# Kernel optimization log

Hardware: AMD Instinct MI355X
Metric: run time of the kernel (lower is better)

Reference implementation:

```python
import jax, jax.numpy as jnp
import numpy as np

G = 4      # groups (conv groups == offset groups)
KS = 3     # kernel size
DIL = 1    # dilation
PAD = 1    # padding = dilation
EPS = 1e-5 # InstanceNorm eps


def setup_inputs() -> dict:
    key = jax.random.key(0)
    k1, k2, k3, k4, k5 = jax.random.split(key, 5)
    B, C, D, H, W = 4, 64, 8, 64, 64
    Cout = 64
    Cg = C // G
    x = jax.random.normal(k1, (B, C, D, H, W), jnp.float32)
    # small offset-conv weights so predicted offsets stay within a few pixels
    w_off = jax.random.normal(k2, (2 * KS * KS * G, Cg, KS, KS), jnp.float32) * 0.01
    b_off = jax.random.normal(k3, (2 * KS * KS * G,), jnp.float32) * 0.01
    w_dc = jax.random.normal(k4, (Cout, Cg, KS, KS), jnp.float32) * (1.0 / np.sqrt(Cg * KS * KS))
    b_dc = jax.random.normal(k5, (Cout,), jnp.float32) * 0.01
    return {"x": x, "w_off": w_off, "b_off": b_off, "w_dc": w_dc, "b_dc": b_dc}


def reference(x, w_off, b_off, w_dc, b_dc):
    B, C, D, H, W = x.shape
    N = B * D
    K = KS * KS
    Cg = C // G
    # torch .view(B*D, C, H, W) is a row-major reshape of the flat buffer
    x2 = x.reshape(N, C, H, W)

    # grouped 3x3 offset conv, same padding
    off = jax.lax.conv_general_dilated(
        x2, w_off, (1, 1), [(PAD, PAD), (PAD, PAD)],
        rhs_dilation=(DIL, DIL), feature_group_count=G,
        dimension_numbers=("NCHW", "OIHW", "NCHW"),
    ) + b_off[None, :, None, None]
    off = off.reshape(N, G, K, 2, H, W)        # (y, x) offset per group/kernel-pt
    dy, dx = off[:, :, :, 0], off[:, :, :, 1]  # [N,G,K,H,W]

    # base sampling grid per kernel point
    ki, kj = jnp.meshgrid(jnp.arange(KS), jnp.arange(KS), indexing="ij")
    ki = ki.reshape(K); kj = kj.reshape(K)
    base_y = (jnp.arange(H)[None, :] - PAD + ki[:, None] * DIL).astype(jnp.float32)  # [K,H]
    base_x = (jnp.arange(W)[None, :] - PAD + kj[:, None] * DIL).astype(jnp.float32)  # [K,W]
    py = base_y[None, None, :, :, None] + dy   # [N,G,K,H,W]
    px = base_x[None, None, :, None, :] + dx

    y0 = jnp.floor(py); x0 = jnp.floor(px)
    ly = py - y0; lx = px - x0
    y0i = y0.astype(jnp.int32); x0i = x0.astype(jnp.int32)

    xg = x2.reshape(N, G, Cg, H * W)
    gather = jax.vmap(jax.vmap(lambda xf, idx: xf[:, idx]))  # over N, G

    def corner(yi, xi, w):
        valid = (yi >= 0) & (yi < H) & (xi >= 0) & (xi < W)   # zero-pad OOB
        idx = jnp.clip(yi, 0, H - 1) * W + jnp.clip(xi, 0, W - 1)
        v = gather(xg, idx.reshape(N, G, -1)).reshape(N, G, Cg, K, H, W)
        return v * (w * valid)[:, :, None]                    # broadcast over Cg

    val = (corner(y0i,     x0i,     (1 - ly) * (1 - lx))
         + corner(y0i,     x0i + 1, (1 - ly) * lx)
         + corner(y0i + 1, x0i,     ly * (1 - lx))
         + corner(y0i + 1, x0i + 1, ly * lx))                 # [N,G,Cg,K,H,W]

    wg = w_dc.reshape(G, -1, Cg, K)                           # [G,Coutg,Cg,K]
    out = jnp.einsum("gock,ngckhw->ngohw", wg, val).reshape(N, -1, H, W)
    out = out + b_dc[None, :, None, None]

    # InstanceNorm2d (affine=False, biased var) + exact GELU
    m = out.mean((-2, -1), keepdims=True)
    v = out.var((-2, -1), keepdims=True)
    out = jax.nn.gelu((out - m) * jax.lax.rsqrt(v + EPS), approximate=False)

    Cout = out.shape[1]
    return out.reshape(B, D, Cout, H, W).transpose(0, 2, 1, 3, 4)  # [B,Cout,D,H,W]
```

## Files before the change

kernel.cpp:

```cpp
#include <hip/hip_runtime.h>
#include <hip/hip_bf16.h>
#include <math.h>

#define HW 4096
#define NN 32
#define W68 68
#define SLICE (68 * 68)

typedef __attribute__((ext_vector_type(8))) short bf16x8;
typedef __attribute__((ext_vector_type(4))) float f32x4;

__device__ inline unsigned short bfbits(float a) {
    __hip_bfloat16 h = __float2bfloat16(a);
    unsigned short u;
    __builtin_memcpy(&u, &h, 2);
    return u;
}
__device__ inline unsigned packbf(float a, float b) {
    return (unsigned)bfbits(a) | ((unsigned)bfbits(b) << 16);
}
__device__ inline float bflo(unsigned u) { return __uint_as_float(u << 16); }
__device__ inline float bfhi(unsigned u) { return __uint_as_float(u & 0xffff0000u); }

__device__ inline int xsw(int x, int c8) {
    return ((x << 5) | (c8 << 4)) ^ (((x >> 2) & 1) << 4);
}

__device__ inline void bilin8(uint4 A, uint4 B, uint4 C, uint4 D,
                              const float* ww, float* val) {
    const unsigned* ua = (const unsigned*)&A;
    const unsigned* ub = (const unsigned*)&B;
    const unsigned* uc = (const unsigned*)&C;
    const unsigned* ud = (const unsigned*)&D;
    #pragma unroll
    for (int j = 0; j < 4; j++) {
        val[2*j]   = ww[0]*bflo(ua[j]) + ww[1]*bflo(ub[j]) + ww[2]*bflo(uc[j]) + ww[3]*bflo(ud[j]);
        val[2*j+1] = ww[0]*bfhi(ua[j]) + ww[1]*bfhi(ub[j]) + ww[2]*bfhi(uc[j]) + ww[3]*bfhi(ud[j]);
    }
}

__global__ __launch_bounds__(256) void transpose_x(const float* __restrict__ x,
                                                   unsigned short* __restrict__ xT,
                                                   const float* __restrict__ w_off,
                                                   const float* __restrict__ w_dc,
                                                   unsigned short* __restrict__ wperm)
{
    int bx = blockIdx.x;
    int t = threadIdx.x;

    if (bx < 120) {
        int idx = bx * 256 + t;
        int g = idx / 7680;
        int r3 = idx - g * 7680;
        int which = r3 / 2560;
        int r = r3 - which * 2560;
        int j = r & 7;
        int rest = r >> 3;
        int nn_ = rest & 15; rest >>= 4;
        int q_ = rest & 3, kp_ = rest >> 2;
        int k = q_ * 8 + j;
        int c = k & 15, tt = kp_ * 2 + (k >> 4);
        float v = 0.f;
        if (tt < 9) {
            if (which == 0)      v = w_dc[(g * 16 + nn_) * 144 + c * 9 + tt];
            else if (which == 1) v = w_off[(g * 18 + nn_) * 144 + c * 9 + tt];
            else if (nn_ < 2)    v = w_off[(g * 18 + 16 + nn_) * 144 + c * 9 + tt];
        }
        wperm[idx] = bfbits(v);
    }

    __shared__ float tile[256 * 17];
    int n = bx >> 6, g = (bx >> 4) & 3, chunk = bx & 15;
    const float* xb = x + (size_t)(n * 64 + g * 16) * HW + chunk * 256;

    #pragma unroll
    for (int r = 0; r < 16; r++) {
        int idx = r * 256 + t;
        int c = idx >> 8, p = idx & 255;
        tile[p * 17 + c] = xb[c * HW + p];
    }
    __syncthreads();

    unsigned short* ob = xT + (size_t)(n * 4 + g) * SLICE * 16;
    #pragma unroll
    for (int r = 0; r < 2; r++) {
        int idx = r * 256 + t;
        int p = idx >> 1, half = idx & 1;
        int pos = chunk * 256 + p;
        int h = pos >> 6, w = pos & 63;
        const float* tp = &tile[p * 17 + half * 8];
        uint4 v;
        v.x = packbf(tp[0], tp[1]);
        v.y = packbf(tp[2], tp[3]);
        v.z = packbf(tp[4], tp[5]);
        v.w = packbf(tp[6], tp[7]);
        *(uint4*)(ob + ((size_t)((h + 2) * W68 + (w + 2)) * 16 + half * 8)) = v;
    }

    if (t < 66) {
        int j = t >> 1, half = t & 1;
        int hp = chunk * 33 + j;
        int R, C;
        if (hp < 136)      { R = hp / 68;               C = hp % 68; }
        else if (hp < 272) { int q2 = hp - 136; R = 66 + q2 / 68; C = q2 % 68; }
        else               { int q2 = hp - 272; R = 2 + (q2 >> 2);
                             C = (q2 & 3); C = C < 2 ? C : C + 64; }
        uint4 z = {0, 0, 0, 0};
        *(uint4*)(ob + ((size_t)(R * W68 + C) * 16 + half * 8)) = z;
    }
}

__global__ __launch_bounds__(256, 4) void fused_conv(const unsigned short* __restrict__ xT,
                                                     const unsigned short* __restrict__ wperm,
                                                     const float* __restrict__ b_off,
                                                     const float* __restrict__ b_dc,
                                                     float* __restrict__ outpre)
{
    __shared__ __attribute__((aligned(16))) unsigned short xwin[9 * 1088];
    __shared__ __attribute__((aligned(8)))  unsigned short off_lds[256 * 20];

    int bx = blockIdx.x;
    int n = bx >> 6, g = (bx >> 4) & 3, chunk = bx & 15;
    int t = threadIdx.x;
    int lane = t & 63, wv = t >> 6;
    int nn = lane & 15, q = lane >> 4;
    int t2 = q >> 1, chh = q & 1;
    int R0 = chunk * 4;

    const unsigned short* wpg = wperm + g * 7680;
    const unsigned short* xsl = xT + (size_t)(n * 4 + g) * SLICE * 16;
    const unsigned short* xw  = xsl + chh * 8;

    {
        uint4 sv[5]; int sof[5];
        #pragma unroll
        for (int k = 0; k < 5; k++) {
            int sidx = k * 256 + t;
            int row = sidx / 136;
            int rem = sidx - row * 136;
            int xx = rem >> 1, c8 = rem & 1;
            int Rg = R0 + row; Rg = Rg > 67 ? 67 : Rg;
            bool ok = sidx < 1224;
            uint4 z = {0, 0, 0, 0};
            sv[k] = ok ? *(const uint4*)(xsl + ((size_t)(Rg * 68 + xx) * 16 + c8 * 8)) : z;
            sof[k] = row * 2176 + xsw(xx, c8);
        }
        #pragma unroll
        for (int k = 0; k < 5; k++) {
            int sidx = k * 256 + t;
            if (sidx < 1224)
                *(uint4*)((char*)xwin + sof[k]) = sv[k];
        }
    }

    int pls[4]; float fy[4], fx[4]; int rws[4], xbs[4];
    #pragma unroll
    for (int s = 0; s < 4; s++) {
        int pl = (wv * 4 + s) * 16 + nn;
        int pos = chunk * 256 + pl;
        int h = pos >> 6, w = pos & 63;
        pls[s] = pl;
        fy[s] = (float)(h - 1);
        fx[s] = (float)(w - 1);
        rws[s] = ((wv * 4 + s) >> 2) + 1;
        xbs[s] = ((wv * 4 + s) & 3) * 16 + nn + 1;
    }

    bf16x8 pb0[5], pb1[5], bwr[5];
    #pragma unroll
    for (int kp = 0; kp < 5; kp++) {
        int fo = ((kp * 4 + q) * 16 + nn) * 8;
        pb0[kp] = *(const bf16x8*)(wpg + 2560 + fo);
        pb1[kp] = *(const bf16x8*)(wpg + 5120 + fo);
        bwr[kp] = *(const bf16x8*)(wpg + fo);
    }

    __syncthreads();

    {
        f32x4 acc0[4], acc1[4];
        float bv0 = b_off[g * 18 + nn];
        float bv1 = (nn < 2) ? b_off[g * 18 + 16 + nn] : 0.f;
        #pragma unroll
        for (int s = 0; s < 4; s++)
            #pragma unroll
            for (int r = 0; r < 4; r++) { acc0[s][r] = bv0; acc1[s][r] = bv1; }

        uint4 xv[2][4];
        auto stage1 = [&](int kp) {
            int ki = t2 ? (2 * kp + 1) / 3 : (2 * kp) / 3;
            int kj = t2 ? (2 * kp + 1) % 3 : (2 * kp) % 3;
            int sl = kp & 1;
            #pragma unroll
            for (int s = 0; s < 4; s++) {
                int adr = (rws[s] + ki) * 2176 + xsw(xbs[s] + kj, chh);
                xv[sl][s] = *(const uint4*)((const char*)xwin + adr);
            }
        };
        stage1(0);
        #pragma unroll
        for (int kp = 0; kp < 5; kp++) {
            if (kp < 4) stage1(kp + 1);
            int sl = kp & 1;
            #pragma unroll
            for (int s = 0; s < 4; s++) {
                bf16x8 af = *(bf16x8*)&xv[sl][s];
                acc0[s] = __builtin_amdgcn_mfma_f32_16x16x32_bf16(af, pb0[kp], acc0[s], 0, 0, 0);
                acc1[s] = __builtin_amdgcn_mfma_f32_16x16x32_bf16(af, pb1[kp], acc1[s], 0, 0, 0);
            }
        }

        #pragma unroll
        for (int s = 0; s < 4; s++) {
            int pl = (wv * 4 + s) * 16 + q * 4;
            #pragma unroll
            for (int r = 0; r < 4; r++) {
                off_lds[(pl + r) * 20 + nn] = bfbits(acc0[s][r]);
                if (nn < 2)
                    off_lds[(pl + r) * 20 + 16 + nn] = bfbits(acc1[s][r]);
            }
        }
        off_lds[t * 20 + 18] = 0;
        off_lds[t * 20 + 19] = 0;
    }
    __syncthreads();

    f32x4 acc[4];
    float bv = b_dc[g * 16 + nn];
    #pragma unroll
    for (int s = 0; s < 4; s++)
        #pragma unroll
        for (int r = 0; r < 4; r++) acc[s][r] = bv;

    uint4 RA[2], RB[2], RC[2], RD[2];
    float rw_[2][4];
    int rinw[2], rgb[2];

    auto stage = [&](int u) {
        int kp = u >> 2, s = u & 3, sl = u & 1;
        int ki = t2 ? (2 * kp + 1) / 3 : (2 * kp) / 3;
        int kj = t2 ? (2 * kp + 1) % 3 : (2 * kp) % 3;
        unsigned uo = *(const unsigned*)&off_lds[pls[s] * 20 + 4 * kp + 2 * t2];
        float py = fy[s] + (float)ki + bflo(uo);
        float px = fx[s] + (float)kj + bfhi(uo);
        float y0f = fminf(fmaxf(floorf(py), -2.f), 64.f);
        float x0f = fminf(fmaxf(floorf(px), -2.f), 64.f);
        float ly = py - y0f, lx = px - x0f;
        float my = 1.f - ly, mx = 1.f - lx;
        rw_[sl][0] = my * mx; rw_[sl][1] = my * lx;
        rw_[sl][2] = ly * mx; rw_[sl][3] = ly * lx;
        int y0 = (int)y0f, x0 = (int)x0f;
        int lr = y0 + 2 - R0;
        int inw = ((unsigned)lr <= 7u);
        int lrc = inw ? lr : 0;
        int xx = x0 + 2;
        int a0 = lrc * 2176 + xsw(xx, chh);
        int a1 = lrc * 2176 + xsw(xx + 1, chh);
        RA[sl] = *(const uint4*)((const char*)xwin + a0);
        RB[sl] = *(const uint4*)((const char*)xwin + a1);
        RC[sl] = *(const uint4*)((const char*)xwin + a0 + 2176);
        RD[sl] = *(const uint4*)((const char*)xwin + a1 + 2176);
        rinw[sl] = inw;
        rgb[sl] = (y0 + 2) * W68 + xx;
    };
    auto consume = [&](int u) {
        int kp = u >> 2, s = u & 3, sl = u & 1;
        if (!__all(rinw[sl])) {
            if (!rinw[sl]) {
                const unsigned short* p0 = xw + (size_t)rgb[sl] * 16;
                RA[sl] = *(const uint4*)(p0);
                RB[sl] = *(const uint4*)(p0 + 16);
                RC[sl] = *(const uint4*)(p0 + W68 * 16);
                RD[sl] = *(const uint4*)(p0 + W68 * 16 + 16);
            }
        }
        float val[8];
        bilin8(RA[sl], RB[sl], RC[sl], RD[sl], rw_[sl], val);
        bf16x8 af;
        #pragma unroll
        for (int j = 0; j < 8; j++) af[j] = (short)bfbits(val[j]);
        acc[s] = __builtin_amdgcn_mfma_f32_16x16x32_bf16(af, bwr[kp], acc[s], 0, 0, 0);
    };

    stage(0);
    #pragma unroll
    for (int u = 0; u < 20; u++) {
        if (u < 19) stage(u + 1);
        consume(u);
    }

    float* op = outpre + (size_t)(n * 64 + g * 16) * HW;
    #pragma unroll
    for (int s = 0; s < 4; s++) {
        int pbase = chunk * 256 + (wv * 4 + s) * 16 + q * 4;
        #pragma unroll
        for (int r = 0; r < 4; r++)
            op[nn * HW + pbase + r] = acc[s][r];
    }
}

__global__ __launch_bounds__(256) void norm_gelu(const float* __restrict__ outpre,
                                                 float* __restrict__ out)
{
    __shared__ float red[8];
    int bx = blockIdx.x;
    int n  = bx >> 6;
    int co = bx & 63;
    int t  = threadIdx.x;

    const float4* base = (const float4*)(outpre + (size_t)(n * 64 + co) * HW);
    float4 v[4];
    float s = 0.f, sq = 0.f;
    #pragma unroll
    for (int r = 0; r < 4; r++) {
        v[r] = base[t + r * 256];
        s  += v[r].x + v[r].y + v[r].z + v[r].w;
        sq  = fmaf(v[r].x, v[r].x, sq);
        sq  = fmaf(v[r].y, v[r].y, sq);
        sq  = fmaf(v[r].z, v[r].z, sq);
        sq  = fmaf(v[r].w, v[r].w, sq);
    }
    #pragma unroll
    for (int o2 = 32; o2 > 0; o2 >>= 1) {
        s  += __shfl_down(s,  o2, 64);
        sq += __shfl_down(sq, o2, 64);
    }
    int wid = t >> 6, lane = t & 63;
    if (lane == 0) { red[wid] = s; red[4 + wid] = sq; }
    __syncthreads();
    float S  = red[0] + red[1] + red[2] + red[3];
    float SQ = red[4] + red[5] + red[6] + red[7];
    float mean = S * (1.f / 4096.f);
    float var  = SQ * (1.f / 4096.f) - mean * mean;
    float rstd = rsqrtf(var + 1e-5f);

    int b = n >> 3, d = n & 7;
    float4* outp = (float4*)(out + ((size_t)(b * 64 + co) * 8 + d) * HW);
    #pragma unroll
    for (int r = 0; r < 4; r++) {
        float xs[4] = {v[r].x, v[r].y, v[r].z, v[r].w};
        float4 res;
        float* rp = (float*)&res;
        #pragma unroll
        for (int qq = 0; qq < 4; qq++) {
            float xn = (xs[qq] - mean) * rstd;
            float u = xn * (1.5957691f + 0.0713548162f * xn * xn);
            float e = __expf(-u);
            rp[qq] = xn * __frcp_rn(1.f + e);
        }
        outp[t + r * 256] = res;
    }
}

extern "C" void kernel_launch(void* const* d_in, const int* in_sizes, int n_in,
                              void* d_out, int out_size, void* d_ws, size_t ws_size,
                              hipStream_t stream) {
    const float* x     = (const float*)d_in[0];
    const float* w_off = (const float*)d_in[1];
    const float* b_off = (const float*)d_in[2];  (void)b_off;
    const float* w_dc  = (const float*)d_in[3];
    const float* b_dc  = (const float*)d_in[4];
    float* out = (float*)d_out;

    unsigned short* wperm = (unsigned short*)d_ws;
    unsigned short* xTb   = wperm + 30720;
    float* outpre = (float*)(xTb + (size_t)NN * 4 * SLICE * 16);


    transpose_x<<<2048, 256, 0, stream>>>(x, xTb, w_off, w_dc, wperm);
    fused_conv <<<2048, 256, 0, stream>>>(xTb, wperm,
                                          (const float*)d_in[2], b_dc, outpre);
    norm_gelu  <<<2048, 256, 0, stream>>>(outpre, out);
}
```

Baseline: 146.8 us.

## Stage input window via direct global-to-LDS loads and defer weight register loads

The input window copy into LDS now uses global_load_lds DMA-style loads instead of staging through registers, with a remapped index computation that matches the swizzled layout. The offset-conv weights are loaded inside the first phase and the deformable-conv weights are loaded after it, which shortens their register live ranges. sched_barrier calls are added to keep the software-pipelined loads ahead of the MFMAs. The changes aim to cut VGPR pressure and load latency, at the risk of layout-mapping errors and padding bytes being written past the old LDS size.

Measured after the change: 135.2 us. 1.09x faster.

```diff
diff --git a/kernel.cpp b/kernel.cpp
--- a/kernel.cpp
+++ b/kernel.cpp
@@ -116,7 +116,7 @@
                                                      const float* __restrict__ b_dc,
                                                      float* __restrict__ outpre)
 {
-    __shared__ __attribute__((aligned(16))) unsigned short xwin[9 * 1088];
+    __shared__ __attribute__((aligned(16))) unsigned short xwin[10240];
     __shared__ __attribute__((aligned(8)))  unsigned short off_lds[256 * 20];
 
     int bx = blockIdx.x;
@@ -132,24 +132,23 @@
     const unsigned short* xw  = xsl + chh * 8;
 
     {
-        uint4 sv[5]; int sof[5];
+        int lane16 = lane * 16;
         #pragma unroll
         for (int k = 0; k < 5; k++) {
-            int sidx = k * 256 + t;
-            int row = sidx / 136;
-            int rem = sidx - row * 136;
-            int xx = rem >> 1, c8 = rem & 1;
+            int ck = wv + k * 4;
+            int d = ck * 1024 + lane16;
+            int row = ((d >> 7) * 241) >> 12;
+            row = row > 8 ? 8 : row;
+            int wr = d - (row << 11) - (row << 7);
+            int x = wr >> 5;
+            x = x > 67 ? 67 : x;
+            int c8 = ((wr >> 4) ^ (wr >> 7)) & 1;
             int Rg = R0 + row; Rg = Rg > 67 ? 67 : Rg;
-            bool ok = sidx < 1224;
-            uint4 z = {0, 0, 0, 0};
-            sv[k] = ok ? *(const uint4*)(xsl + ((size_t)(Rg * 68 + xx) * 16 + c8 * 8)) : z;
-            sof[k] = row * 2176 + xsw(xx, c8);
-        }
-        #pragma unroll
-        for (int k = 0; k < 5; k++) {
-            int sidx = k * 256 + t;
-            if (sidx < 1224)
-                *(uint4*)((char*)xwin + sof[k]) = sv[k];
+            const unsigned short* gp = xsl + ((size_t)(Rg * 68 + x) * 16 + c8 * 8);
+            __builtin_amdgcn_global_load_lds(
+                (const __attribute__((address_space(1))) void*)gp,
+                (__attribute__((address_space(3))) void*)((char*)xwin + ck * 1024),
+                16, 0, 0);
         }
     }
 
@@ -166,18 +165,17 @@
         xbs[s] = ((wv * 4 + s) & 3) * 16 + nn + 1;
     }
 
-    bf16x8 pb0[5], pb1[5], bwr[5];
-    #pragma unroll
-    for (int kp = 0; kp < 5; kp++) {
-        int fo = ((kp * 4 + q) * 16 + nn) * 8;
-        pb0[kp] = *(const bf16x8*)(wpg + 2560 + fo);
-        pb1[kp] = *(const bf16x8*)(wpg + 5120 + fo);
-        bwr[kp] = *(const bf16x8*)(wpg + fo);
-    }
-
     __syncthreads();
 
     {
+        bf16x8 pb0[5], pb1[5];
+        #pragma unroll
+        for (int kp = 0; kp < 5; kp++) {
+            int fo = ((kp * 4 + q) * 16 + nn) * 8;
+            pb0[kp] = *(const bf16x8*)(wpg + 2560 + fo);
+            pb1[kp] = *(const bf16x8*)(wpg + 5120 + fo);
+        }
+
         f32x4 acc0[4], acc1[4];
         float bv0 = b_off[g * 18 + nn];
         float bv1 = (nn < 2) ? b_off[g * 18 + 16 + nn] : 0.f;
@@ -201,6 +199,7 @@
         #pragma unroll
         for (int kp = 0; kp < 5; kp++) {
             if (kp < 4) stage1(kp + 1);
+            __builtin_amdgcn_sched_barrier(0);
             int sl = kp & 1;
             #pragma unroll
             for (int s = 0; s < 4; s++) {
@@ -223,6 +222,12 @@
         off_lds[t * 20 + 18] = 0;
         off_lds[t * 20 + 19] = 0;
     }
+
+    bf16x8 bwr[5];
+    #pragma unroll
+    for (int kp = 0; kp < 5; kp++)
+        bwr[kp] = *(const bf16x8*)(wpg + ((kp * 4 + q) * 16 + nn) * 8);
+
     __syncthreads();
 
     f32x4 acc[4];
@@ -286,6 +291,7 @@
     #pragma unroll
     for (int u = 0; u < 20; u++) {
         if (u < 19) stage(u + 1);
+        __builtin_amdgcn_sched_barrier(0);
         consume(u);
     }
 
```
